# Kernel tuning notes

Hardware: AMD Instinct MI355X
Metric: run time of the kernel (lower is better)

## Reference

```python
import jax, jax.numpy as jnp
import numpy as np

B, IN, HID, OUT = 1024, 512, 128, 64
INP1 = IN + 1  # 513, after prepending ones column


def setup_inputs() -> dict:
    key = jax.random.key(0)
    k1, k2, k3, k4, k5, k6, k7, k8 = jax.random.split(key, 8)
    s1 = 1.0 / np.sqrt(INP1 * INP1)
    s2 = 1.0 / np.sqrt(HID)
    return {
        "img": jax.random.normal(k1, (B, IN), dtype=jnp.float32),
        "tab": jax.random.normal(k2, (B, IN), dtype=jnp.float32),
        "W1": jax.random.uniform(k3, (HID, INP1 * INP1), jnp.float32, -s1, s1),
        "b1": jax.random.uniform(k4, (HID,), jnp.float32, -s1, s1),
        "W2": jax.random.uniform(k5, (HID, HID), jnp.float32, -s2, s2),
        "b2": jax.random.uniform(k6, (HID,), jnp.float32, -s2, s2),
        "W3": jax.random.uniform(k7, (OUT, HID), jnp.float32, -s2, s2),
        "b3": jax.random.uniform(k8, (OUT,), jnp.float32, -s2, s2),
    }


def reference(img, tab, W1, b1, W2, b2, W3, b3):
    ones = jnp.ones((img.shape[0], 1), dtype=img.dtype)
    x = jnp.concatenate([ones, img], axis=1)  # [B, IN+1]
    t = jnp.concatenate([ones, tab], axis=1)  # [B, IN+1]
    # batched outer product, flattened: [B, (IN+1)*(IN+1)]
    fusion = jnp.einsum("bi,bj->bij", x, t).reshape(x.shape[0], -1)
    # dropout is identity in eval mode
    y1 = fusion @ W1.T + b1
    y2 = jnp.tanh(y1 @ W2.T + b2)
    y3 = jax.nn.relu(y2 @ W3.T + b3)
    return y3
```

## Files before the change

kernel.cpp:

```cpp
#include <hip/hip_runtime.h>
#include <hip/hip_bf16.h>

typedef __bf16 bf16x8 __attribute__((ext_vector_type(8)));
typedef float f32x4 __attribute__((ext_vector_type(4)));
typedef unsigned short u16x8 __attribute__((ext_vector_type(8)));

typedef __attribute__((address_space(1))) const unsigned int gu32;
typedef __attribute__((address_space(3))) unsigned int lu32;

#define B_SZ   1024
#define IN_SZ  512
#define HID    128
#define OUT_SZ 64
#define BM     64
#define BN     512
#define BK     32
#define NKT    16

static __device__ __forceinline__ unsigned short f2bf(float f) {
    __hip_bfloat16 h = __float2bfloat16(f);
    return *reinterpret_cast<unsigned short*>(&h);
}

__global__ __launch_bounds__(256) void prep_kernel(
    const float* __restrict__ img, const float* __restrict__ tab,
    unsigned short* __restrict__ tbt, float* __restrict__ xhT,
    float* __restrict__ tc)
{
    const int blk = blockIdx.x;
    for (int j = threadIdx.x; j < 512; j += 256) {
        float v = (j == 0) ? 1.0f : tab[(size_t)blk * IN_SZ + (j - 1)];
        tbt[(size_t)blk * 512 + j] = f2bf(v);
    }
    if (threadIdx.x == 0) tc[blk] = tab[(size_t)blk * IN_SZ + 511];
    if (blk < 513) {
        for (int b = threadIdx.x; b < B_SZ; b += 256)
            xhT[(size_t)blk * B_SZ + b] =
                (blk == 0) ? 1.0f : img[(size_t)b * IN_SZ + (blk - 1)];
    }
}

__global__ __launch_bounds__(512, 4) void gemm_fused(
    const float* __restrict__ w1, const unsigned short* __restrict__ tbt,
    const float* __restrict__ xhT, const float* __restrict__ tc,
    float* __restrict__ y1acc)
{
    __shared__ float          Afs[2][BM * BK];
    __shared__ unsigned short Bls[2][BN * BK];

    const int bm = blockIdx.x >> 1;
    const int bn = blockIdx.x & 1;
    const int m0 = bm * BM;
    const int n0 = bn * BN;
    const int tid  = threadIdx.x;
    const int wv   = tid >> 6;
    const int lane = tid & 63;
    const int l15  = lane & 15;
    const int kg   = lane >> 4;

    const int ar  = tid >> 3;
    const int acl = (tid & 7) ^ (ar & 7);
    const float* asrc = w1 + (size_t)(m0 + ar) * 513 + acl * 4;
    const int aBase = (wv * 64) * 4;

    const unsigned short* bsrc[4];
    int bBase[4];
    #pragma unroll
    for (int q = 0; q < 4; ++q) {
        const int p  = q * 512 + tid;
        const int r  = p >> 2;
        const int cl = (p & 3) ^ ((r >> 1) & 3);
        bsrc[q] = tbt + (size_t)(n0 + r) * 512 + cl * 8;
        bBase[q] = (q * 512 + wv * 64) * 8;
    }

    int aoff0[4], aoff1[4], boffs[4];
    #pragma unroll
    for (int ms = 0; ms < 4; ++ms) {
        const int r = ms * 16 + l15;
        aoff0[ms] = r * 32 + (((kg * 2) + 0) ^ (r & 7)) * 4;
        aoff1[ms] = r * 32 + (((kg * 2) + 1) ^ (r & 7)) * 4;
    }
    #pragma unroll
    for (int ns = 0; ns < 4; ++ns) {
        const int r = wv * 64 + ns * 16 + l15;
        boffs[ns] = ((r << 2) | (kg ^ ((r >> 1) & 3))) * 8;
    }

    f32x4 acc[4][4] = {};

#define STAGE(BUF, KT) do {                                                  \
        const int k32_ = (KT) * BK;                                          \
        _Pragma("unroll")                                                    \
        for (int q_ = 0; q_ < 4; ++q_)                                       \
            __builtin_amdgcn_global_load_lds(                                \
                (gu32*)(const void*)(bsrc[q_] + k32_),                       \
                (lu32*)(void*)&Bls[BUF][bBase[q_]], 16, 0, 0);               \
        __builtin_amdgcn_global_load_lds(                                    \
            (gu32*)(const void*)(asrc + k32_),                               \
            (lu32*)(void*)&Afs[BUF][aBase], 16, 0, 0);                       \
    } while (0)

    STAGE(0, 0);
    __syncthreads();

    for (int kt = 0; kt < NKT; ++kt) {
        const int cur = kt & 1;
        if (kt + 1 < NKT) STAGE(cur ^ 1, kt + 1);

        const float*          ab = &Afs[cur][0];
        const unsigned short* bb = &Bls[cur][0];

        bf16x8 bfr[4];
        #pragma unroll
        for (int ns = 0; ns < 4; ++ns)
            bfr[ns] = *reinterpret_cast<const bf16x8*>(&bb[boffs[ns]]);

        #pragma unroll
        for (int ms = 0; ms < 4; ++ms) {
            const f32x4 lo = *reinterpret_cast<const f32x4*>(&ab[aoff0[ms]]);
            const f32x4 hi = *reinterpret_cast<const f32x4*>(&ab[aoff1[ms]]);
            u16x8 u;
            u[0] = f2bf(lo[0]); u[1] = f2bf(lo[1]);
            u[2] = f2bf(lo[2]); u[3] = f2bf(lo[3]);
            u[4] = f2bf(hi[0]); u[5] = f2bf(hi[1]);
            u[6] = f2bf(hi[2]); u[7] = f2bf(hi[3]);
            const bf16x8 af = __builtin_bit_cast(bf16x8, u);
            #pragma unroll
            for (int ns = 0; ns < 4; ++ns)
                acc[ms][ns] = __builtin_amdgcn_mfma_f32_16x16x32_bf16(
                    af, bfr[ns], acc[ms][ns], 0, 0, 0);
        }
        __syncthreads();
    }
#undef STAGE

    const int h0 = m0 / 513;
    const int mb = (h0 + 1) * 513;
    const bool cross = (mb < m0 + BM);

    float wc[4][4];
    #pragma unroll
    for (int ms = 0; ms < 4; ++ms)
        #pragma unroll
        for (int v = 0; v < 4; ++v)
            wc[ms][v] = w1[(size_t)(m0 + ms * 16 + kg * 4 + v) * 513 + 512];

    #pragma unroll
    for (int ns = 0; ns < 4; ++ns) {
        const int ncol = n0 + wv * 64 + ns * 16 + l15;
        const float tv = tc[ncol];
        float s0 = 0.f, s1 = 0.f;
        #pragma unroll
        for (int ms = 0; ms < 4; ++ms) {
            #pragma unroll
            for (int v = 0; v < 4; ++v) {
                const int m = m0 + ms * 16 + kg * 4 + v;
                const bool lo = (m < mb);
                const int i = lo ? (m - h0 * 513) : (m - mb);
                const float xv = xhT[(size_t)i * B_SZ + ncol];
                const float val = (acc[ms][ns][v] + wc[ms][v] * tv) * xv;
                if (lo) s0 += val; else s1 += val;
            }
        }
        s0 += __shfl_xor(s0, 16); s0 += __shfl_xor(s0, 32);
        if (lane < 16) atomicAdd(&y1acc[(size_t)ncol * HID + h0], s0);
        if (cross) {
            s1 += __shfl_xor(s1, 16); s1 += __shfl_xor(s1, 32);
            if (lane < 16 && (h0 + 1) < HID)
                atomicAdd(&y1acc[(size_t)ncol * HID + h0 + 1], s1);
        }
    }
}

__global__ __launch_bounds__(128) void mlp_kernel(
    const float* __restrict__ y1acc, const float* __restrict__ b1,
    const float* __restrict__ W2, const float* __restrict__ b2,
    const float* __restrict__ W3, const float* __restrict__ b3,
    float* __restrict__ out)
{
    __shared__ float y1r[HID];
    __shared__ float y2r[HID];
    const int b = blockIdx.x;
    const int h = threadIdx.x;
    y1r[h] = y1acc[(size_t)b * HID + h] + b1[h];
    __syncthreads();
    float a = b2[h];
    const float* w2r = W2 + (size_t)h * HID;
    #pragma unroll 8
    for (int k = 0; k < HID; ++k) a += w2r[k] * y1r[k];
    y2r[h] = tanhf(a);
    __syncthreads();
    if (h < OUT_SZ) {
        float a3 = b3[h];
        const float* w3r = W3 + (size_t)h * HID;
        #pragma unroll 8
        for (int k = 0; k < HID; ++k) a3 += w3r[k] * y2r[k];
        out[(size_t)b * OUT_SZ + h] = fmaxf(a3, 0.f);
    }
}

extern "C" void kernel_launch(void* const* d_in, const int* in_sizes, int n_in,
                              void* d_out, int out_size, void* d_ws, size_t ws_size,
                              hipStream_t stream) {
    const float* img = (const float*)d_in[0];
    const float* tab = (const float*)d_in[1];
    const float* W1  = (const float*)d_in[2];
    const float* b1  = (const float*)d_in[3];
    const float* W2  = (const float*)d_in[4];
    const float* b2  = (const float*)d_in[5];
    const float* W3  = (const float*)d_in[6];
    const float* b3  = (const float*)d_in[7];
    float* out = (float*)d_out;

    char* ws = (char*)d_ws;
    float*          y1acc = (float*)ws;
    unsigned short* tbt   = (unsigned short*)(ws + 524288);
    float*          xhT   = (float*)(ws + 1572864);
    float*          tc    = (float*)(ws + 3674112);

    hipMemsetAsync(y1acc, 0, (size_t)B_SZ * HID * sizeof(float), stream);
    prep_kernel<<<dim3(1024), dim3(256), 0, stream>>>(img, tab, tbt, xhT, tc);
    gemm_fused<<<dim3(2052), dim3(512), 0, stream>>>(W1, tbt, xhT, tc, y1acc);
    mlp_kernel<<<dim3(1024), dim3(128), 0, stream>>>(y1acc, b1, W2, b2, W3, b3, out);
}
```

Measured before the change: 201.4 us.

## Pre-convert W1 to bf16 and use 128x256 GEMM tiles with bf16 A staging

A new pre-pass converts the fp32 W1 into a packed bf16 copy in the workspace, 512 columns per row. The main GEMM can then stage A directly as bf16 and drop the per-iteration fp32-to-bf16 conversion in the inner loop. Block tiles change from 64x512 to 128x256 with a 2x4 wave layout, which rebalances A/B reuse. The cost is an extra full read of W1 plus a 67 MB write on every call, which may outweigh the cheaper inner loop. The original kernel is kept as a fallback for when the workspace is too small.

```diff
diff --git a/kernel.cpp b/kernel.cpp
--- a/kernel.cpp
+++ b/kernel.cpp
@@ -3,6 +3,7 @@
 
 typedef __bf16 bf16x8 __attribute__((ext_vector_type(8)));
 typedef float f32x4 __attribute__((ext_vector_type(4)));
+typedef float f32x4u __attribute__((ext_vector_type(4), aligned(4)));
 typedef unsigned short u16x8 __attribute__((ext_vector_type(8)));
 
 typedef __attribute__((address_space(1))) const unsigned int gu32;
@@ -12,8 +13,6 @@
 #define IN_SZ  512
 #define HID    128
 #define OUT_SZ 64
-#define BM     64
-#define BN     512
 #define BK     32
 #define NKT    16
 
@@ -40,18 +39,163 @@
     }
 }
 
+__global__ __launch_bounds__(256) void prep2_kernel(
+    const float* __restrict__ w1, unsigned short* __restrict__ w1b)
+{
+    const long long gid = (long long)blockIdx.x * 256 + threadIdx.x;
+    const int r  = (int)(gid >> 6);
+    const int c8 = ((int)gid & 63) << 3;
+    const float* src = w1 + (size_t)r * 513 + c8;
+    const f32x4u lo = *reinterpret_cast<const f32x4u*>(src);
+    const f32x4u hi = *reinterpret_cast<const f32x4u*>(src + 4);
+    u16x8 u;
+    u[0] = f2bf(lo[0]); u[1] = f2bf(lo[1]); u[2] = f2bf(lo[2]); u[3] = f2bf(lo[3]);
+    u[4] = f2bf(hi[0]); u[5] = f2bf(hi[1]); u[6] = f2bf(hi[2]); u[7] = f2bf(hi[3]);
+    *reinterpret_cast<u16x8*>(w1b + (size_t)r * 512 + c8) = u;
+}
+
 __global__ __launch_bounds__(512, 4) void gemm_fused(
+    const float* __restrict__ w1, const unsigned short* __restrict__ w1b,
+    const unsigned short* __restrict__ tbt,
+    const float* __restrict__ xhT, const float* __restrict__ tc,
+    float* __restrict__ y1acc)
+{
+    __shared__ unsigned short Als[2][128 * BK];
+    __shared__ unsigned short Bls[2][256 * BK];
+
+    const int bm = blockIdx.x >> 2;
+    const int bn = blockIdx.x & 3;
+    const int m0 = bm * 128;
+    const int n0 = bn * 256;
+    const int tid  = threadIdx.x;
+    const int wv   = tid >> 6;
+    const int wr   = wv >> 2;
+    const int wc   = wv & 3;
+    const int lane = tid & 63;
+    const int l15  = lane & 15;
+    const int kg   = lane >> 4;
+
+    const unsigned short* asrc;
+    {
+        const int r  = tid >> 2;
+        const int cl = (tid & 3) ^ ((r >> 1) & 3);
+        asrc = w1b + (size_t)(m0 + r) * 512 + cl * 8;
+    }
+    const int aBase = (wv * 64) * 8;
+
+    const unsigned short* bsrc[2];
+    int bBase[2];
+    #pragma unroll
+    for (int q = 0; q < 2; ++q) {
+        const int p  = q * 512 + tid;
+        const int r  = p >> 2;
+        const int cl = (p & 3) ^ ((r >> 1) & 3);
+        bsrc[q] = tbt + (size_t)(n0 + r) * 512 + cl * 8;
+        bBase[q] = (q * 512 + wv * 64) * 8;
+    }
+
+    int aoffs[4], boffs[4];
+    #pragma unroll
+    for (int ms = 0; ms < 4; ++ms) {
+        const int r = wr * 64 + ms * 16 + l15;
+        aoffs[ms] = (r * 4 + (kg ^ ((r >> 1) & 3))) * 8;
+    }
+    #pragma unroll
+    for (int ns = 0; ns < 4; ++ns) {
+        const int r = wc * 64 + ns * 16 + l15;
+        boffs[ns] = (r * 4 + (kg ^ ((r >> 1) & 3))) * 8;
+    }
+
+    f32x4 acc[4][4] = {};
+
+#define STAGE(BUF, KT) do {                                                  \
+        const int k32_ = (KT) * BK;                                          \
+        __builtin_amdgcn_global_load_lds(                                    \
+            (gu32*)(const void*)(asrc + k32_),                               \
+            (lu32*)(void*)&Als[BUF][aBase], 16, 0, 0);                       \
+        _Pragma("unroll")                                                    \
+        for (int q_ = 0; q_ < 2; ++q_)                                       \
+            __builtin_amdgcn_global_load_lds(                                \
+                (gu32*)(const void*)(bsrc[q_] + k32_),                       \
+                (lu32*)(void*)&Bls[BUF][bBase[q_]], 16, 0, 0);               \
+    } while (0)
+
+    STAGE(0, 0);
+    __syncthreads();
+
+    for (int kt = 0; kt < NKT; ++kt) {
+        const int cur = kt & 1;
+        if (kt + 1 < NKT) STAGE(cur ^ 1, kt + 1);
+
+        const unsigned short* ab = &Als[cur][0];
+        const unsigned short* bb = &Bls[cur][0];
+        bf16x8 af[4], bfr[4];
+        #pragma unroll
+        for (int ms = 0; ms < 4; ++ms)
+            af[ms] = *reinterpret_cast<const bf16x8*>(&ab[aoffs[ms]]);
+        #pragma unroll
+        for (int ns = 0; ns < 4; ++ns)
+            bfr[ns] = *reinterpret_cast<const bf16x8*>(&bb[boffs[ns]]);
+        #pragma unroll
+        for (int ms = 0; ms < 4; ++ms)
+            #pragma unroll
+            for (int ns = 0; ns < 4; ++ns)
+                acc[ms][ns] = __builtin_amdgcn_mfma_f32_16x16x32_bf16(
+                    af[ms], bfr[ns], acc[ms][ns], 0, 0, 0);
+        __syncthreads();
+    }
+#undef STAGE
+
+    const int h0 = m0 / 513;
+    const int mb = (h0 + 1) * 513;
+    const bool cross = (mb < m0 + 128);
+
+    float wcv[4][4];
+    #pragma unroll
+    for (int ms = 0; ms < 4; ++ms)
+        #pragma unroll
+        for (int v = 0; v < 4; ++v)
+            wcv[ms][v] = w1[(size_t)(m0 + wr * 64 + ms * 16 + kg * 4 + v) * 513 + 512];
+
+    #pragma unroll
+    for (int ns = 0; ns < 4; ++ns) {
+        const int ncol = n0 + wc * 64 + ns * 16 + l15;
+        const float tv = tc[ncol];
+        float s0 = 0.f, s1 = 0.f;
+        #pragma unroll
+        for (int ms = 0; ms < 4; ++ms) {
+            #pragma unroll
+            for (int v = 0; v < 4; ++v) {
+                const int m = m0 + wr * 64 + ms * 16 + kg * 4 + v;
+                const bool lo = (m < mb);
+                const int i = lo ? (m - h0 * 513) : (m - mb);
+                const float xv = xhT[(size_t)i * B_SZ + ncol];
+                const float val = (acc[ms][ns][v] + wcv[ms][v] * tv) * xv;
+                if (lo) s0 += val; else s1 += val;
+            }
+        }
+        s0 += __shfl_xor(s0, 16); s0 += __shfl_xor(s0, 32);
+        if (lane < 16) atomicAdd(&y1acc[(size_t)ncol * HID + h0], s0);
+        if (cross) {
+            s1 += __shfl_xor(s1, 16); s1 += __shfl_xor(s1, 32);
+            if (lane < 16 && (h0 + 1) < HID)
+                atomicAdd(&y1acc[(size_t)ncol * HID + h0 + 1], s1);
+        }
+    }
+}
+
+__global__ __launch_bounds__(512, 4) void gemm_fused_fb(
     const float* __restrict__ w1, const unsigned short* __restrict__ tbt,
     const float* __restrict__ xhT, const float* __restrict__ tc,
     float* __restrict__ y1acc)
 {
-    __shared__ float          Afs[2][BM * BK];
-    __shared__ unsigned short Bls[2][BN * BK];
+    __shared__ float          Afs[2][64 * BK];
+    __shared__ unsigned short Bls[2][512 * BK];
 
     const int bm = blockIdx.x >> 1;
     const int bn = blockIdx.x & 1;
-    const int m0 = bm * BM;
-    const int n0 = bn * BN;
+    const int m0 = bm * 64;
+    const int n0 = bn * 512;
     const int tid  = threadIdx.x;
     const int wv   = tid >> 6;
     const int lane = tid & 63;
@@ -89,7 +233,7 @@
 
     f32x4 acc[4][4] = {};
 
-#define STAGE(BUF, KT) do {                                                  \
+#define STAGE_FB(BUF, KT) do {                                               \
         const int k32_ = (KT) * BK;                                          \
         _Pragma("unroll")                                                    \
         for (int q_ = 0; q_ < 4; ++q_)                                       \
@@ -101,21 +245,19 @@
             (lu32*)(void*)&Afs[BUF][aBase], 16, 0, 0);                       \
     } while (0)
 
-    STAGE(0, 0);
+    STAGE_FB(0, 0);
     __syncthreads();
 
     for (int kt = 0; kt < NKT; ++kt) {
         const int cur = kt & 1;
-        if (kt + 1 < NKT) STAGE(cur ^ 1, kt + 1);
+        if (kt + 1 < NKT) STAGE_FB(cur ^ 1, kt + 1);
 
         const float*          ab = &Afs[cur][0];
         const unsigned short* bb = &Bls[cur][0];
-
         bf16x8 bfr[4];
         #pragma unroll
         for (int ns = 0; ns < 4; ++ns)
             bfr[ns] = *reinterpret_cast<const bf16x8*>(&bb[boffs[ns]]);
-
         #pragma unroll
         for (int ms = 0; ms < 4; ++ms) {
             const f32x4 lo = *reinterpret_cast<const f32x4*>(&ab[aoff0[ms]]);
@@ -133,18 +275,18 @@
         }
         __syncthreads();
     }
-#undef STAGE
+#undef STAGE_FB
 
     const int h0 = m0 / 513;
     const int mb = (h0 + 1) * 513;
-    const bool cross = (mb < m0 + BM);
-
-    float wc[4][4];
+    const bool cross = (mb < m0 + 64);
+
+    float wcv[4][4];
     #pragma unroll
     for (int ms = 0; ms < 4; ++ms)
         #pragma unroll
         for (int v = 0; v < 4; ++v)
-            wc[ms][v] = w1[(size_t)(m0 + ms * 16 + kg * 4 + v) * 513 + 512];
+            wcv[ms][v] = w1[(size_t)(m0 + ms * 16 + kg * 4 + v) * 513 + 512];
 
     #pragma unroll
     for (int ns = 0; ns < 4; ++ns) {
@@ -159,7 +301,7 @@
                 const bool lo = (m < mb);
                 const int i = lo ? (m - h0 * 513) : (m - mb);
                 const float xv = xhT[(size_t)i * B_SZ + ncol];
-                const float val = (acc[ms][ns][v] + wc[ms][v] * tv) * xv;
+                const float val = (acc[ms][ns][v] + wcv[ms][v] * tv) * xv;
                 if (lo) s0 += val; else s1 += val;
             }
         }
@@ -218,9 +360,16 @@
     unsigned short* tbt   = (unsigned short*)(ws + 524288);
     float*          xhT   = (float*)(ws + 1572864);
     float*          tc    = (float*)(ws + 3674112);
+    unsigned short* w1b   = (unsigned short*)(ws + 3678208);
+    const size_t need = 3678208ULL + 67239936ULL;
 
     hipMemsetAsync(y1acc, 0, (size_t)B_SZ * HID * sizeof(float), stream);
     prep_kernel<<<dim3(1024), dim3(256), 0, stream>>>(img, tab, tbt, xhT, tc);
-    gemm_fused<<<dim3(2052), dim3(512), 0, stream>>>(W1, tbt, xhT, tc, y1acc);
+    if (ws_size >= need) {
+        prep2_kernel<<<dim3(65664 * 64 / 256), dim3(256), 0, stream>>>(W1, w1b);
+        gemm_fused<<<dim3(2052), dim3(512), 0, stream>>>(W1, w1b, tbt, xhT, tc, y1acc);
+    } else {
+        gemm_fused_fb<<<dim3(2052), dim3(512), 0, stream>>>(W1, tbt, xhT, tc, y1acc);
+    }
     mlp_kernel<<<dim3(1024), dim3(128), 0, stream>>>(y1acc, b1, W2, b2, W3, b3, out);
 }
```

New measurement: 205.9 us. 1.02x slower.
